# Optimization experiments

Measured on AMD Instinct MI355X. Metric: run time of the kernel, lower is better.

## Reference

```python
import jax, jax.numpy as jnp
import numpy as np
from jax.scipy.special import erf

DIM = 8  # Cl(3,0) multivector dimension
BV_IDX = jnp.array([3, 5, 6])  # blades with popcount==2 in bitmask ordering
GRADES = np.array([bin(i).count('1') for i in range(DIM)])
GRADES_J = jnp.asarray(GRADES)
REV_SIGN = jnp.asarray(np.where((GRADES * (GRADES - 1) // 2) % 2 == 0, 1.0, -1.0).astype(np.float32))


def _cayley():
    # Geometric-product structure tensor for Cl(3,0): (e_a e_b) = sign * e_{a^b}
    C = np.zeros((DIM, DIM, DIM), dtype=np.float32)
    for a in range(DIM):
        for b in range(DIM):
            s, t = 0, a >> 1
            while t:
                s += bin(t & b).count('1')
                t >>= 1
            C[a, b, a ^ b] = -1.0 if (s & 1) else 1.0
    return jnp.asarray(C)

CAYLEY = _cayley()


def rotor_exp(bv):
    # bv: [..., 3] bivector coefficients -> rotor multivector [..., 8]
    # B^2 = -|B|^2 in Cl(3,0), so exp(B) = cos|B| + sin|B|/|B| * B
    theta = jnp.sqrt(jnp.sum(bv * bv, axis=-1, keepdims=True))
    sinc = jnp.where(theta > 1e-6, jnp.sin(theta) / jnp.maximum(theta, 1e-6), 1.0)
    R = jnp.zeros(bv.shape[:-1] + (DIM,), bv.dtype)
    R = R.at[..., 0].set(jnp.cos(theta)[..., 0])
    R = R.at[..., BV_IDX].set(sinc * bv)
    return R


def reverse(x):
    return x * REV_SIGN


def setup_inputs() -> dict:
    key = jax.random.key(0)
    ks = jax.random.split(key, 8)
    B, C, A = 65536, 32, 5
    return {
        'state': jax.random.normal(ks[0], (B, C, DIM), jnp.float32),
        'action': jax.random.randint(ks[1], (B,), 0, A),
        'action_bivectors': 0.1 * jax.random.normal(ks[2], (A, 3), jnp.float32),
        'norm_scale': jnp.ones((C,), jnp.float32),
        'rotor_bv': 0.1 * jax.random.normal(ks[3], (C, 3), jnp.float32),
        'lin_W': jax.random.normal(ks[4], (C, C, 4), jnp.float32) / np.sqrt(C),
        'lin_b': jnp.zeros((C,), jnp.float32),
        'reward_W': jax.random.normal(ks[5], (1, C), jnp.float32) / np.sqrt(C),
        'reward_b': jnp.zeros((1,), jnp.float32),
    }


def reference(state, action, action_bivectors, norm_scale, rotor_bv, lin_W, lin_b, reward_W, reward_b):
    # 1-2. gather action bivector, rotor R = exp(-B/2)
    bv = -0.5 * action_bivectors[action]                 # [B, 3]
    R = rotor_exp(bv)                                    # [B, 8]
    Rr = reverse(R)
    # 3. sandwich s' = R s R~ per channel
    t = jnp.einsum('bi,bcj,ijk->bck', R, state, CAYLEY)
    x = jnp.einsum('bck,bl,klm->bcm', t, Rr, CAYLEY)     # [B, C, 8]
    # 4. GA refine block (residual)
    # CliffordLayerNorm: per-channel multivector norm + learnable scale
    n = jnp.sqrt(jnp.sum(x * x, axis=-1, keepdims=True) + 1e-6)
    h = x / n * norm_scale[None, :, None]
    # GeometricGELU: gate whole multivector by Phi(scalar part)
    gate = 0.5 * (1.0 + erf(h[..., :1] * jnp.asarray(0.7071067811865476, h.dtype)))
    h = h * gate
    # RotorLayer: per-channel learned rotor sandwich
    Rc = rotor_exp(-0.5 * rotor_bv)                      # [C, 8]
    Rcr = reverse(Rc)
    t2 = jnp.einsum('ci,bcj,ijk->bck', Rc, h, CAYLEY)
    h = jnp.einsum('bck,cl,klm->bcm', t2, Rcr, CAYLEY)
    # CliffordLinear: grade-wise channel mixing
    Wg = lin_W[:, :, GRADES_J]                           # [C_out, C_in, 8]
    h = jnp.einsum('bid,oid->bod', h, Wg)
    h = h.at[..., 0].add(lin_b)
    next_state = x + h
    # 5. reward from grade-0
    reward = next_state[:, :, 0] @ reward_W.T + reward_b  # [B, 1]
    return reward, next_state
```

## Files before the change

kernel.cpp:

```cpp
#include <hip/hip_runtime.h>
#include <hip/hip_bf16.h>

typedef __bf16 bf16x8 __attribute__((ext_vector_type(8)));
typedef float  floatx4 __attribute__((ext_vector_type(4)));

__device__ __forceinline__ __bf16 to_bf16(float f) {
    unsigned int u = __builtin_bit_cast(unsigned int, f);
    u += 0x7FFFu + ((u >> 16) & 1u);
    unsigned short h = (unsigned short)(u >> 16);
    return __builtin_bit_cast(__bf16, h);
}

__host__ __device__ constexpr float csign(int a, int b) {
    int s = 0;
    for (int k = 1; k < 4; ++k) {
        int t = (a >> k) & b;
        s += (t & 1) + ((t >> 1) & 1) + ((t >> 2) & 1);
    }
    return (s & 1) ? -1.0f : 1.0f;
}

__device__ __forceinline__ void rotor_sandwich(const float r[4], const float s_in[8], float x[8]) {
    constexpr int RI[4] = {0, 3, 5, 6};
    float t[8];
#pragma unroll
    for (int k = 0; k < 8; ++k) t[k] = 0.f;
#pragma unroll
    for (int ia = 0; ia < 4; ++ia) {
#pragma unroll
        for (int jb = 0; jb < 8; ++jb) {
            t[RI[ia] ^ jb] += csign(RI[ia], jb) * r[ia] * s_in[jb];
        }
    }
    const float rr[4] = {r[0], -r[1], -r[2], -r[3]};
#pragma unroll
    for (int k = 0; k < 8; ++k) x[k] = 0.f;
#pragma unroll
    for (int ka = 0; ka < 8; ++ka) {
#pragma unroll
        for (int ib = 0; ib < 4; ++ib) {
            x[ka ^ RI[ib]] += csign(ka, RI[ib]) * t[ka] * rr[ib];
        }
    }
}

__device__ __forceinline__ void rotor_from_bv(float b0, float b1, float b2, float r[4]) {
    float t2 = b0 * b0 + b1 * b1 + b2 * b2;
    float th = sqrtf(t2);
    float sc = (th > 1e-6f) ? (__sinf(th) / th) : 1.0f;
    r[0] = __cosf(th);
    r[1] = sc * b0;
    r[2] = sc * b1;
    r[3] = sc * b2;
}

__global__ __launch_bounds__(64, 2) void dyn_kernel(
    const float* __restrict__ state, const int* __restrict__ action,
    const float* __restrict__ act_bv, const float* __restrict__ norm_scale,
    const float* __restrict__ rotor_bv, const float* __restrict__ lin_W,
    const float* __restrict__ lin_b, const float* __restrict__ reward_W,
    const float* __restrict__ reward_b,
    float* __restrict__ out_reward, float* __restrict__ out_next)
{
    const int lane = threadIdx.x;
    const int bl = lane & 15;
    const int q  = lane >> 4;
    const int b  = blockIdx.x * 16 + bl;

    __shared__ float h2s[8 * 16 * 36];

    float r[4];
    {
        const int a = action[b];
        const float* p = act_bv + a * 3;
        rotor_from_bv(-0.5f * p[0], -0.5f * p[1], -0.5f * p[2], r);
    }

    const float* sp = state + ((size_t)b * 32 + (size_t)q * 8) * 8;
    float4 sv[8][2];
#pragma unroll
    for (int j = 0; j < 8; ++j) {
        sv[j][0] = ((const float4*)sp)[j * 2 + 0];
        sv[j][1] = ((const float4*)sp)[j * 2 + 1];
    }

    float  x[8][8];
    bf16x8 afrag[8];

#pragma unroll
    for (int j = 0; j < 8; ++j) {
        const int c = q * 8 + j;
        float s_in[8] = {sv[j][0].x, sv[j][0].y, sv[j][0].z, sv[j][0].w,
                         sv[j][1].x, sv[j][1].y, sv[j][1].z, sv[j][1].w};
        float xv[8];
        rotor_sandwich(r, s_in, xv);

        float ss = 1e-6f;
#pragma unroll
        for (int d = 0; d < 8; ++d) ss += xv[d] * xv[d];
        float hscale = norm_scale[c] * rsqrtf(ss);
        float h0 = xv[0] * hscale;
        float gate = 0.5f * (1.0f + erff(h0 * 0.70710678118654752440f));
        float g2 = hscale * gate;

        float hv[8];
#pragma unroll
        for (int d = 0; d < 8; ++d) hv[d] = xv[d] * g2;

        float rc[4];
        {
            const float* rp = rotor_bv + c * 3;
            rotor_from_bv(-0.5f * rp[0], -0.5f * rp[1], -0.5f * rp[2], rc);
        }
        float hf[8];
        rotor_sandwich(rc, hv, hf);

#pragma unroll
        for (int d = 0; d < 8; ++d) {
            x[j][d] = xv[d];
            afrag[d][j] = to_bf16(hf[d]);
        }
    }

    bf16x8 bfrag[4][2];
#pragma unroll
    for (int hh = 0; hh < 2; ++hh) {
        const int o = bl + 16 * hh;
#pragma unroll
        for (int j = 0; j < 8; ++j) {
            const int i = q * 8 + j;
            float4 w = ((const float4*)lin_W)[o * 32 + i];
            bfrag[0][hh][j] = to_bf16(w.x);
            bfrag[1][hh][j] = to_bf16(w.y);
            bfrag[2][hh][j] = to_bf16(w.z);
            bfrag[3][hh][j] = to_bf16(w.w);
        }
    }

    constexpr int GR[8] = {0, 1, 1, 2, 1, 2, 2, 3};
    floatx4 acc[8][2];
#pragma unroll
    for (int d = 0; d < 8; ++d) {
#pragma unroll
        for (int hh = 0; hh < 2; ++hh) {
            floatx4 z = {0.f, 0.f, 0.f, 0.f};
            acc[d][hh] = __builtin_amdgcn_mfma_f32_16x16x32_bf16(
                afrag[d], bfrag[GR[d]][hh], z, 0, 0, 0);
        }
    }

#pragma unroll
    for (int hh = 0; hh < 2; ++hh) {
        const float lb = lin_b[bl + 16 * hh];
#pragma unroll
        for (int rg = 0; rg < 4; ++rg) acc[0][hh][rg] += lb;
    }

#pragma unroll
    for (int d = 0; d < 8; ++d) {
#pragma unroll
        for (int hh = 0; hh < 2; ++hh) {
            const int o = bl + 16 * hh;
#pragma unroll
            for (int rg = 0; rg < 4; ++rg) {
                const int row = q * 4 + rg;
                h2s[d * 576 + row * 36 + o] = acc[d][hh][rg];
            }
        }
    }
    __syncthreads();

#pragma unroll
    for (int d = 0; d < 8; ++d) {
        const float* hp = &h2s[d * 576 + bl * 36 + q * 8];
        float4 ha = ((const float4*)hp)[0];
        float4 hb = ((const float4*)hp)[1];
        x[0][d] += ha.x; x[1][d] += ha.y; x[2][d] += ha.z; x[3][d] += ha.w;
        x[4][d] += hb.x; x[5][d] += hb.y; x[6][d] += hb.z; x[7][d] += hb.w;
    }

    float* op = out_next + ((size_t)b * 32 + (size_t)q * 8) * 8;
    float rsum = 0.f;
#pragma unroll
    for (int j = 0; j < 8; ++j) {
        rsum += x[j][0] * reward_W[q * 8 + j];
        float4 o0 = {x[j][0], x[j][1], x[j][2], x[j][3]};
        float4 o1 = {x[j][4], x[j][5], x[j][6], x[j][7]};
        ((float4*)op)[j * 2 + 0] = o0;
        ((float4*)op)[j * 2 + 1] = o1;
    }
    rsum += __shfl_xor(rsum, 16, 64);
    rsum += __shfl_xor(rsum, 32, 64);
    if (q == 0) out_reward[b] = rsum + reward_b[0];
}

extern "C" void kernel_launch(void* const* d_in, const int* in_sizes, int n_in,
                              void* d_out, int out_size, void* d_ws, size_t ws_size,
                              hipStream_t stream) {
    const float* state      = (const float*)d_in[0];
    const int*   action     = (const int*)  d_in[1];
    const float* act_bv     = (const float*)d_in[2];
    const float* norm_scale = (const float*)d_in[3];
    const float* rotor_bv   = (const float*)d_in[4];
    const float* lin_W      = (const float*)d_in[5];
    const float* lin_b      = (const float*)d_in[6];
    const float* reward_W   = (const float*)d_in[7];
    const float* reward_b   = (const float*)d_in[8];

    float* out = (float*)d_out;
    const int B = in_sizes[1];
    float* out_reward = out;
    float* out_next   = out + B;

    dim3 grid(B / 16), block(64);
    hipLaunchKernelGGL(dyn_kernel, grid, block, 0, stream,
                       state, action, act_bv, norm_scale, rotor_bv,
                       lin_W, lin_b, reward_W, reward_b, out_reward, out_next);
    (void)n_in; (void)out_size; (void)d_ws; (void)ws_size;
}
```

Measured before the change: 154.9 us.

## Fold residual into MFMA via identity operand and drop LDS transpose

The residual x is now added inside the matrix unit: x goes in as a second bf16 A-fragment multiplied by an identity B-fragment, and the bias is preloaded into the accumulator. Output is written straight from the MFMA register layout, which removes the shared-memory transpose, the barrier and the held fp32 x registers. The work runs in two passes of four blades to cut register pressure, with 256-thread blocks holding four independent waves. In exchange, the residual path loses precision because x is rounded to bf16, and the output stores become 16-byte strided chunks instead of contiguous per-lane runs.

Result: slower. 175.1 us (+13.0%).

```diff
diff --git a/kernel.cpp b/kernel.cpp
--- a/kernel.cpp
+++ b/kernel.cpp
@@ -5,7 +5,7 @@
 typedef float  floatx4 __attribute__((ext_vector_type(4)));
 
 __device__ __forceinline__ __bf16 to_bf16(float f) {
-    unsigned int u = __builtin_bit_cast(unsigned int, f);
+    unsigned u = __builtin_bit_cast(unsigned, f);
     u += 0x7FFFu + ((u >> 16) & 1u);
     unsigned short h = (unsigned short)(u >> 16);
     return __builtin_bit_cast(__bf16, h);
@@ -54,7 +54,30 @@
     r[3] = sc * b2;
 }
 
-__global__ __launch_bounds__(64, 2) void dyn_kernel(
+__device__ __forceinline__ void channel_fwd(const float r[4], float nsc,
+                                            const float* __restrict__ rbv,
+                                            float4 s0, float4 s1,
+                                            float* xo, float* hf) {
+    float s_in[8] = {s0.x, s0.y, s0.z, s0.w, s1.x, s1.y, s1.z, s1.w};
+    float xv[8];
+    rotor_sandwich(r, s_in, xv);
+    float ss = 1e-6f;
+#pragma unroll
+    for (int d = 0; d < 8; ++d) ss += xv[d] * xv[d];
+    float hscale = nsc * rsqrtf(ss);
+    float gate = 0.5f * (1.0f + erff(xv[0] * hscale * 0.70710678118654752440f));
+    float g2 = hscale * gate;
+    float hv[8];
+#pragma unroll
+    for (int d = 0; d < 8; ++d) hv[d] = xv[d] * g2;
+    float rc[4];
+    rotor_from_bv(-0.5f * rbv[0], -0.5f * rbv[1], -0.5f * rbv[2], rc);
+    rotor_sandwich(rc, hv, hf);
+#pragma unroll
+    for (int d = 0; d < 8; ++d) xo[d] = xv[d];
+}
+
+__global__ __launch_bounds__(256, 3) void dyn_kernel(
     const float* __restrict__ state, const int* __restrict__ action,
     const float* __restrict__ act_bv, const float* __restrict__ norm_scale,
     const float* __restrict__ rotor_bv, const float* __restrict__ lin_W,
@@ -62,12 +85,14 @@
     const float* __restrict__ reward_b,
     float* __restrict__ out_reward, float* __restrict__ out_next)
 {
-    const int lane = threadIdx.x;
-    const int bl = lane & 15;
-    const int q  = lane >> 4;
-    const int b  = blockIdx.x * 16 + bl;
-
-    __shared__ float h2s[8 * 16 * 36];
+    const int tid   = threadIdx.x;
+    const int lane  = tid & 63;
+    const int wv    = tid >> 6;
+    const int bl    = lane & 15;
+    const int q     = lane >> 4;
+    const int bbase = blockIdx.x * 64 + wv * 16;
+    const int b     = bbase + bl;
+    const int cbase = 8 * q;
 
     float r[4];
     {
@@ -76,122 +101,101 @@
         rotor_from_bv(-0.5f * p[0], -0.5f * p[1], -0.5f * p[2], r);
     }
 
-    const float* sp = state + ((size_t)b * 32 + (size_t)q * 8) * 8;
-    float4 sv[8][2];
-#pragma unroll
-    for (int j = 0; j < 8; ++j) {
-        sv[j][0] = ((const float4*)sp)[j * 2 + 0];
-        sv[j][1] = ((const float4*)sp)[j * 2 + 1];
-    }
-
-    float  x[8][8];
-    bf16x8 afrag[8];
-
-#pragma unroll
-    for (int j = 0; j < 8; ++j) {
-        const int c = q * 8 + j;
-        float s_in[8] = {sv[j][0].x, sv[j][0].y, sv[j][0].z, sv[j][0].w,
-                         sv[j][1].x, sv[j][1].y, sv[j][1].z, sv[j][1].w};
-        float xv[8];
-        rotor_sandwich(r, s_in, xv);
-
-        float ss = 1e-6f;
-#pragma unroll
-        for (int d = 0; d < 8; ++d) ss += xv[d] * xv[d];
-        float hscale = norm_scale[c] * rsqrtf(ss);
-        float h0 = xv[0] * hscale;
-        float gate = 0.5f * (1.0f + erff(h0 * 0.70710678118654752440f));
-        float g2 = hscale * gate;
-
-        float hv[8];
-#pragma unroll
-        for (int d = 0; d < 8; ++d) hv[d] = xv[d] * g2;
-
-        float rc[4];
-        {
-            const float* rp = rotor_bv + c * 3;
-            rotor_from_bv(-0.5f * rp[0], -0.5f * rp[1], -0.5f * rp[2], rc);
-        }
-        float hf[8];
-        rotor_sandwich(rc, hv, hf);
-
+    bf16x8 ah[8];
+    bf16x8 ax[8];
+    const float* sp = state + ((size_t)b * 32 + cbase) * 8;
+#pragma unroll
+    for (int i = 0; i < 4; ++i) {
+        const int cA = cbase + 2 * i, cB = cA + 1;
+        float4 sa0 = ((const float4*)sp)[4 * i + 0];
+        float4 sa1 = ((const float4*)sp)[4 * i + 1];
+        float4 sb0 = ((const float4*)sp)[4 * i + 2];
+        float4 sb1 = ((const float4*)sp)[4 * i + 3];
+        float xa[8], ha[8], xb[8], hb[8];
+        channel_fwd(r, norm_scale[cA], rotor_bv + cA * 3, sa0, sa1, xa, ha);
+        channel_fwd(r, norm_scale[cB], rotor_bv + cB * 3, sb0, sb1, xb, hb);
 #pragma unroll
         for (int d = 0; d < 8; ++d) {
-            x[j][d] = xv[d];
-            afrag[d][j] = to_bf16(hf[d]);
-        }
-    }
-
-    bf16x8 bfrag[4][2];
-#pragma unroll
-    for (int hh = 0; hh < 2; ++hh) {
-        const int o = bl + 16 * hh;
-#pragma unroll
-        for (int j = 0; j < 8; ++j) {
-            const int i = q * 8 + j;
-            float4 w = ((const float4*)lin_W)[o * 32 + i];
-            bfrag[0][hh][j] = to_bf16(w.x);
-            bfrag[1][hh][j] = to_bf16(w.y);
-            bfrag[2][hh][j] = to_bf16(w.z);
-            bfrag[3][hh][j] = to_bf16(w.w);
-        }
-    }
+            ah[d][2 * i]     = to_bf16(ha[d]);
+            ah[d][2 * i + 1] = to_bf16(hb[d]);
+            ax[d][2 * i]     = to_bf16(xa[d]);
+            ax[d][2 * i + 1] = to_bf16(xb[d]);
+        }
+    }
+
+    const __bf16 one_bf  = __builtin_bit_cast(__bf16, (unsigned short)0x3F80);
+    const __bf16 zero_bf = __builtin_bit_cast(__bf16, (unsigned short)0x0000);
+    bf16x8 BI[2];
+#pragma unroll
+    for (int hh = 0; hh < 2; ++hh)
+#pragma unroll
+        for (int j = 0; j < 8; ++j)
+            BI[hh][j] = (cbase + j == bl + 16 * hh) ? one_bf : zero_bf;
+
+    const float lb[2] = {lin_b[bl], lin_b[bl + 16]};
 
     constexpr int GR[8] = {0, 1, 1, 2, 1, 2, 2, 3};
-    floatx4 acc[8][2];
-#pragma unroll
-    for (int d = 0; d < 8; ++d) {
-#pragma unroll
-        for (int hh = 0; hh < 2; ++hh) {
-            floatx4 z = {0.f, 0.f, 0.f, 0.f};
-            acc[d][hh] = __builtin_amdgcn_mfma_f32_16x16x32_bf16(
-                afrag[d], bfrag[GR[d]][hh], z, 0, 0, 0);
-        }
-    }
-
-#pragma unroll
-    for (int hh = 0; hh < 2; ++hh) {
-        const float lb = lin_b[bl + 16 * hh];
-#pragma unroll
-        for (int rg = 0; rg < 4; ++rg) acc[0][hh][rg] += lb;
-    }
-
-#pragma unroll
-    for (int d = 0; d < 8; ++d) {
+    float r4[4] = {0.f, 0.f, 0.f, 0.f};
+
+#pragma unroll
+    for (int pass = 0; pass < 2; ++pass) {
+        bf16x8 Wf[4][2];
 #pragma unroll
         for (int hh = 0; hh < 2; ++hh) {
             const int o = bl + 16 * hh;
 #pragma unroll
+            for (int j = 0; j < 8; ++j) {
+                float4 w = ((const float4*)lin_W)[o * 32 + cbase + j];
+                Wf[0][hh][j] = to_bf16(w.x);
+                Wf[1][hh][j] = to_bf16(w.y);
+                Wf[2][hh][j] = to_bf16(w.z);
+                Wf[3][hh][j] = to_bf16(w.w);
+            }
+        }
+
+        floatx4 acc[4][2];
+#pragma unroll
+        for (int dd = 0; dd < 4; ++dd) {
+            const int d = pass * 4 + dd;
+#pragma unroll
+            for (int hh = 0; hh < 2; ++hh) {
+                floatx4 c0;
+                const float ci = (d == 0) ? lb[hh] : 0.f;
+                c0[0] = ci; c0[1] = ci; c0[2] = ci; c0[3] = ci;
+                floatx4 t = __builtin_amdgcn_mfma_f32_16x16x32_bf16(ah[d], Wf[GR[d]][hh], c0, 0, 0, 0);
+                acc[dd][hh]  = __builtin_amdgcn_mfma_f32_16x16x32_bf16(ax[d], BI[hh],     t,  0, 0, 0);
+            }
+        }
+
+        if (pass == 0) {
+            const float rwlo = reward_W[bl], rwhi = reward_W[bl + 16];
+#pragma unroll
+            for (int rg = 0; rg < 4; ++rg)
+                r4[rg] = acc[0][0][rg] * rwlo + acc[0][1][rg] * rwhi;
+        }
+
+#pragma unroll
+        for (int hh = 0; hh < 2; ++hh) {
+#pragma unroll
             for (int rg = 0; rg < 4; ++rg) {
-                const int row = q * 4 + rg;
-                h2s[d * 576 + row * 36 + o] = acc[d][hh][rg];
+                float* dst = out_next +
+                    ((size_t)(bbase + 4 * q + rg) * 32 + (bl + 16 * hh)) * 8 + 4 * pass;
+                float4 v = {acc[0][hh][rg], acc[1][hh][rg], acc[2][hh][rg], acc[3][hh][rg]};
+                *(float4*)dst = v;
             }
         }
     }
-    __syncthreads();
-
-#pragma unroll
-    for (int d = 0; d < 8; ++d) {
-        const float* hp = &h2s[d * 576 + bl * 36 + q * 8];
-        float4 ha = ((const float4*)hp)[0];
-        float4 hb = ((const float4*)hp)[1];
-        x[0][d] += ha.x; x[1][d] += ha.y; x[2][d] += ha.z; x[3][d] += ha.w;
-        x[4][d] += hb.x; x[5][d] += hb.y; x[6][d] += hb.z; x[7][d] += hb.w;
-    }
-
-    float* op = out_next + ((size_t)b * 32 + (size_t)q * 8) * 8;
-    float rsum = 0.f;
-#pragma unroll
-    for (int j = 0; j < 8; ++j) {
-        rsum += x[j][0] * reward_W[q * 8 + j];
-        float4 o0 = {x[j][0], x[j][1], x[j][2], x[j][3]};
-        float4 o1 = {x[j][4], x[j][5], x[j][6], x[j][7]};
-        ((float4*)op)[j * 2 + 0] = o0;
-        ((float4*)op)[j * 2 + 1] = o1;
-    }
-    rsum += __shfl_xor(rsum, 16, 64);
-    rsum += __shfl_xor(rsum, 32, 64);
-    if (q == 0) out_reward[b] = rsum + reward_b[0];
+
+#pragma unroll
+    for (int m = 1; m <= 8; m <<= 1) {
+#pragma unroll
+        for (int rg = 0; rg < 4; ++rg)
+            r4[rg] += __shfl_xor(r4[rg], m, 64);
+    }
+    if (bl < 4) {
+        float v = (bl == 0) ? r4[0] : (bl == 1) ? r4[1] : (bl == 2) ? r4[2] : r4[3];
+        out_reward[bbase + 4 * q + bl] = v + reward_b[0];
+    }
 }
 
 extern "C" void kernel_launch(void* const* d_in, const int* in_sizes, int n_in,
@@ -212,7 +216,7 @@
     float* out_reward = out;
     float* out_next   = out + B;
 
-    dim3 grid(B / 16), block(64);
+    dim3 grid(B / 64), block(256);
     hipLaunchKernelGGL(dyn_kernel, grid, block, 0, stream,
                        state, action, act_bv, norm_scale, rotor_bv,
                        lin_W, lin_b, reward_W, reward_b, out_reward, out_next);
```
